# Kernel optimization log

Measured on AMD Instinct MI355X. Metric: run time of the kernel, lower is better.

The kernel has to match this reference:

```python
import jax, jax.numpy as jnp
import numpy as np

N = 8192
IN_DIM = 128
OUT_DIM = 64
ALPHA = 0.2  # leaky_relu negative slope
NEG_BIG = -9e15


def setup_inputs() -> dict:
    key = jax.random.key(0)
    k1, k2, k3, k4, k5 = jax.random.split(key, 5)
    h = jax.random.normal(k1, (N, IN_DIM), dtype=jnp.float32)
    adj = jax.random.randint(k2, (N, N), 0, 2, dtype=jnp.int32)
    w = jax.random.normal(k3, (IN_DIM, OUT_DIM), dtype=jnp.float32) * (1.414 / np.sqrt(IN_DIM))
    a = jax.random.normal(k4, (2 * OUT_DIM, 1), dtype=jnp.float32) * 0.1
    b = jax.random.uniform(k5, (OUT_DIM,), dtype=jnp.float32, minval=-1.0, maxval=1.0) / np.sqrt(OUT_DIM)
    return {"h": h, "adj": adj, "w": w, "a": a, "b": b}


def reference(h, adj, w, a, b):
    # wh: [N, D_out]
    wh = h @ w
    d = wh.shape[1]
    # broadcast attention logits: e[i,j] = leaky_relu(wh[i]@a1 + wh[j]@a2)
    wh1 = wh @ a[:d]   # [N, 1]
    wh2 = wh @ a[d:]   # [N, 1]
    e = jax.nn.leaky_relu(wh1 + wh2.T, negative_slope=ALPHA)  # [N, N]
    # adjacency mask + row softmax (dropout=0 / eval mode -> identity)
    att = jnp.where(adj > 0, e, NEG_BIG)
    att = jax.nn.softmax(att, axis=1)
    h_prime = att @ wh + b  # [N, D_out]
    return jax.nn.elu(h_prime)  # concat=True -> elu
```

## Files before the change

kernel.cpp:

```cpp
#include <hip/hip_runtime.h>
#include <hip/hip_bf16.h>

#define NN 8192
#define D_IN 128
#define D_OUT 64
#define GAT_ALPHA 0.2f
#define LOG2E 1.4426950408889634f

typedef __attribute__((ext_vector_type(4))) float f32x4;
typedef __attribute__((ext_vector_type(8))) short short8;

static __device__ __forceinline__ unsigned short f32_bf16(float f) {
    unsigned u = __builtin_bit_cast(unsigned, f);
    u += 0x7fffu + ((u >> 16) & 1u);
    return (unsigned short)(u >> 16);
}

__global__ __launch_bounds__(256) void gat_pre(
    const int* __restrict__ adj, unsigned char* __restrict__ bm,
    const float* __restrict__ h, const float* __restrict__ w,
    const float* __restrict__ a,
    unsigned short* __restrict__ whB, float* __restrict__ wh1p,
    float* __restrict__ wh2p)
{
    __shared__ float hs[16 * 128];
    __shared__ float whs[16][64];
    const int t = threadIdx.x;

    if (blockIdx.x < 2048) {
        const size_t base = (size_t)blockIdx.x * 256 + t;
        #pragma unroll
        for (int it = 0; it < 16; ++it) {
            const size_t G = (size_t)it * 524288 + base;
            const int4* p = (const int4*)(adj + G * 8);
            int4 v0 = p[0], v1 = p[1];
            unsigned b = 0;
            b |= (unsigned)(v0.x > 0) << 0;
            b |= (unsigned)(v0.y > 0) << 1;
            b |= (unsigned)(v0.z > 0) << 2;
            b |= (unsigned)(v0.w > 0) << 3;
            b |= (unsigned)(v1.x > 0) << 4;
            b |= (unsigned)(v1.y > 0) << 5;
            b |= (unsigned)(v1.z > 0) << 6;
            b |= (unsigned)(v1.w > 0) << 7;
            bm[G] = (unsigned char)b;
        }
        return;
    }

    const int i0 = (blockIdx.x - 2048) * 16;

    const float* hsrc = h + (size_t)i0 * D_IN;
    *(float4*)(hs + t * 8)     = *(const float4*)(hsrc + t * 8);
    *(float4*)(hs + t * 8 + 4) = *(const float4*)(hsrc + t * 8 + 4);
    __syncthreads();

    const int r  = t >> 4;
    const int og = (t & 15) * 4;
    f32x4 acc = {0.f, 0.f, 0.f, 0.f};
    for (int k = 0; k < D_IN; ++k) {
        float hv = hs[r * 128 + k];
        float4 wv = *(const float4*)(w + k * D_OUT + og);
        acc[0] += hv * wv.x; acc[1] += hv * wv.y;
        acc[2] += hv * wv.z; acc[3] += hv * wv.w;
    }
    whs[r][og]     = acc[0];
    whs[r][og + 1] = acc[1];
    whs[r][og + 2] = acc[2];
    whs[r][og + 3] = acc[3];

    float p1 = acc[0]*a[og] + acc[1]*a[og+1] + acc[2]*a[og+2] + acc[3]*a[og+3];
    float p2 = acc[0]*a[64+og] + acc[1]*a[64+og+1] + acc[2]*a[64+og+2] + acc[3]*a[64+og+3];
    #pragma unroll
    for (int m = 1; m < 16; m <<= 1) {
        p1 += __shfl_xor(p1, m);
        p2 += __shfl_xor(p2, m);
    }
    if ((t & 15) == 0) {
        wh1p[i0 + r] = p1 * LOG2E;
        wh2p[i0 + r] = p2 * LOG2E;
    }
    __syncthreads();

    {
        const int half = t >> 7;
        const int dim  = (t >> 1) & 63;
        const int e0   = (t & 1) * 4;
        ushort4 v;
        v.x = f32_bf16(whs[half * 8 + e0 + 0][dim]);
        v.y = f32_bf16(whs[half * 8 + e0 + 1][dim]);
        v.z = f32_bf16(whs[half * 8 + e0 + 2][dim]);
        v.w = f32_bf16(whs[half * 8 + e0 + 3][dim]);
        *(ushort4*)(whB + (size_t)(i0 / 8 + half) * 512 + dim * 8 + e0) = v;
    }
}

static __device__ __forceinline__ short8 pack8_bf16(const float* p) {
    union { unsigned int u[4]; short8 s; } r;
    asm("v_cvt_pk_bf16_f32 %0, %1, %2" : "=v"(r.u[0]) : "v"(p[0]), "v"(p[1]));
    asm("v_cvt_pk_bf16_f32 %0, %1, %2" : "=v"(r.u[1]) : "v"(p[2]), "v"(p[3]));
    asm("v_cvt_pk_bf16_f32 %0, %1, %2" : "=v"(r.u[2]) : "v"(p[4]), "v"(p[5]));
    asm("v_cvt_pk_bf16_f32 %0, %1, %2" : "=v"(r.u[3]) : "v"(p[6]), "v"(p[7]));
    return r.s;
}

__global__ __launch_bounds__(512) void gat_main(
    const unsigned int* __restrict__ bm, const unsigned short* __restrict__ whB,
    const float* __restrict__ wh1p, const float* __restrict__ wh2p,
    const float* __restrict__ bias, float* __restrict__ out)
{
    __shared__ alignas(16) char smem[66560];
    unsigned int (*bmlds)[260] = (unsigned int(*)[260])smem;
    float* w2lds = (float*)(smem + 33280);
    float (*nums)[32][64] = (float(*)[32][64])smem;
    float (*dens)[32] = (float(*)[32])(smem + 65536);

    const int t    = threadIdx.x;
    const int wv   = t >> 6;
    const int lane = t & 63;
    const int il   = lane & 15;
    const int kg   = lane >> 4;
    const int r0   = blockIdx.x * 32;

    {
        const uint4*  bmg = (const uint4*)(bm + r0 * 256);
        const float4* w2g = (const float4*)wh2p;
        #pragma unroll
        for (int q = 0; q < 4; ++q) {
            const int C = q * 512 + t;
            uint4 v = bmg[C];
            const int rr = C >> 6, cc = (C & 63) * 4;
            *(uint4*)&bmlds[rr][cc] = v;
            float4 wv2 = w2g[C];
            *(float4*)&w2lds[C * 4] = wv2;
        }
    }
    __syncthreads();

    const float c0 = wh1p[r0 + il];
    const float c1 = wh1p[r0 + 16 + il];
    const int shk = kg * 8;

    f32x4 acc[2][4] = {};
    float den0 = 0.f, den1 = 0.f;

    #pragma unroll 4
    for (int n = 0; n < 32; ++n) {
        const int jd = wv * 32 + n;
        const int j0 = jd * 32;

        unsigned int m0 = bmlds[il][jd] >> shk;
        unsigned int m1 = bmlds[16 + il][jd] >> shk;
        float4 W0 = *(const float4*)&w2lds[j0 + kg * 8];
        float4 W1 = *(const float4*)&w2lds[j0 + kg * 8 + 4];

        const unsigned short* bb = whB + (size_t)(j0 / 8 + kg) * 512 + il * 8;
        short8 b0 = *(const short8*)(bb);
        short8 b1 = *(const short8*)(bb + 128);
        short8 b2 = *(const short8*)(bb + 256);
        short8 b3 = *(const short8*)(bb + 384);

        float wvv[8] = {W0.x, W0.y, W0.z, W0.w, W1.x, W1.y, W1.z, W1.w};
        float p0[8], p1[8];
        #pragma unroll
        for (int e = 0; e < 8; ++e) {
            float x = c0 + wvv[e];
            x = fmaxf(x, GAT_ALPHA * x);
            float p = __builtin_amdgcn_exp2f(x);
            p = (m0 & (1u << e)) ? p : 0.f;
            den0 += p; p0[e] = p;
            float y = c1 + wvv[e];
            y = fmaxf(y, GAT_ALPHA * y);
            float q = __builtin_amdgcn_exp2f(y);
            q = (m1 & (1u << e)) ? q : 0.f;
            den1 += q; p1[e] = q;
        }
        short8 af0 = pack8_bf16(p0);
        short8 af1 = pack8_bf16(p1);

        acc[0][0] = __builtin_amdgcn_mfma_f32_16x16x32_bf16(af0, b0, acc[0][0], 0, 0, 0);
        acc[1][0] = __builtin_amdgcn_mfma_f32_16x16x32_bf16(af1, b0, acc[1][0], 0, 0, 0);
        acc[0][1] = __builtin_amdgcn_mfma_f32_16x16x32_bf16(af0, b1, acc[0][1], 0, 0, 0);
        acc[1][1] = __builtin_amdgcn_mfma_f32_16x16x32_bf16(af1, b1, acc[1][1], 0, 0, 0);
        acc[0][2] = __builtin_amdgcn_mfma_f32_16x16x32_bf16(af0, b2, acc[0][2], 0, 0, 0);
        acc[1][2] = __builtin_amdgcn_mfma_f32_16x16x32_bf16(af1, b2, acc[1][2], 0, 0, 0);
        acc[0][3] = __builtin_amdgcn_mfma_f32_16x16x32_bf16(af0, b3, acc[0][3], 0, 0, 0);
        acc[1][3] = __builtin_amdgcn_mfma_f32_16x16x32_bf16(af1, b3, acc[1][3], 0, 0, 0);
    }

    den0 += __shfl_xor(den0, 16); den0 += __shfl_xor(den0, 32);
    den1 += __shfl_xor(den1, 16); den1 += __shfl_xor(den1, 32);

    __syncthreads();

    if (kg == 0) { dens[wv][il] = den0; dens[wv][16 + il] = den1; }
    #pragma unroll
    for (int q = 0; q < 4; ++q) {
        #pragma unroll
        for (int d = 0; d < 4; ++d) {
            nums[wv][kg * 4 + q][d * 16 + il]      = acc[0][d][q];
            nums[wv][16 + kg * 4 + q][d * 16 + il] = acc[1][d][q];
        }
    }
    __syncthreads();

    #pragma unroll
    for (int k = 0; k < 4; ++k) {
        const int idx = k * 512 + t;
        const int rr = idx >> 6, cc = idx & 63;
        float s = 0.f, dd = 0.f;
        #pragma unroll
        for (int w8 = 0; w8 < 8; ++w8) { s += nums[w8][rr][cc]; dd += dens[w8][rr]; }
        float val = s / dd + bias[cc];
        out[(size_t)(r0 + rr) * D_OUT + cc] =
            val > 0.f ? val : (__builtin_amdgcn_exp2f(val * LOG2E) - 1.f);
    }
}

extern "C" void kernel_launch(void* const* d_in, const int* in_sizes, int n_in,
                              void* d_out, int out_size, void* d_ws, size_t ws_size,
                              hipStream_t stream) {
    const float* h   = (const float*)d_in[0];
    const int*   adj = (const int*)d_in[1];
    const float* w   = (const float*)d_in[2];
    const float* a   = (const float*)d_in[3];
    const float* b   = (const float*)d_in[4];
    float* out = (float*)d_out;

    char* ws = (char*)d_ws;
    unsigned short* whB = (unsigned short*)ws;
    float* wh1p = (float*)(ws + (size_t)D_OUT * NN * 2);
    float* wh2p = (float*)(ws + (size_t)D_OUT * NN * 2 + NN * 4);
    unsigned char* bm = (unsigned char*)(ws + (size_t)D_OUT * NN * 2 + NN * 8);

    gat_pre<<<2560, 256, 0, stream>>>(adj, bm, h, w, a, whB, wh1p, wh2p);
    gat_main<<<256, 512, 0, stream>>>((const unsigned int*)bm, whB, wh1p, wh2p, b, out);
}
```

Baseline: 79.41 us.

## Fuse adjacency bitmask packing into main attention kernel with 16-row tiles

Moves the int32 adjacency-to-bitmask conversion out of the prep kernel and into the main kernel. Each block now streams its own adjacency rows with nontemporal loads and packs them into LDS, which avoids writing and re-reading a global bitmask. The main kernel is retiled to 16 rows per block with 512 blocks, and wh2 is read straight from global memory instead of being staged in LDS. In exchange the 256MB adjacency read now sits inside the compute kernel, and whB is reused across half as many rows per block.

```diff
diff --git a/kernel.cpp b/kernel.cpp
--- a/kernel.cpp
+++ b/kernel.cpp
@@ -9,6 +9,7 @@
 
 typedef __attribute__((ext_vector_type(4))) float f32x4;
 typedef __attribute__((ext_vector_type(8))) short short8;
+typedef __attribute__((ext_vector_type(4))) int i32x4;
 
 static __device__ __forceinline__ unsigned short f32_bf16(float f) {
     unsigned u = __builtin_bit_cast(unsigned, f);
@@ -16,8 +17,7 @@
     return (unsigned short)(u >> 16);
 }
 
-__global__ __launch_bounds__(256) void gat_pre(
-    const int* __restrict__ adj, unsigned char* __restrict__ bm,
+__global__ __launch_bounds__(256) void gat_prep(
     const float* __restrict__ h, const float* __restrict__ w,
     const float* __restrict__ a,
     unsigned short* __restrict__ whB, float* __restrict__ wh1p,
@@ -26,29 +26,7 @@
     __shared__ float hs[16 * 128];
     __shared__ float whs[16][64];
     const int t = threadIdx.x;
-
-    if (blockIdx.x < 2048) {
-        const size_t base = (size_t)blockIdx.x * 256 + t;
-        #pragma unroll
-        for (int it = 0; it < 16; ++it) {
-            const size_t G = (size_t)it * 524288 + base;
-            const int4* p = (const int4*)(adj + G * 8);
-            int4 v0 = p[0], v1 = p[1];
-            unsigned b = 0;
-            b |= (unsigned)(v0.x > 0) << 0;
-            b |= (unsigned)(v0.y > 0) << 1;
-            b |= (unsigned)(v0.z > 0) << 2;
-            b |= (unsigned)(v0.w > 0) << 3;
-            b |= (unsigned)(v1.x > 0) << 4;
-            b |= (unsigned)(v1.y > 0) << 5;
-            b |= (unsigned)(v1.z > 0) << 6;
-            b |= (unsigned)(v1.w > 0) << 7;
-            bm[G] = (unsigned char)b;
-        }
-        return;
-    }
-
-    const int i0 = (blockIdx.x - 2048) * 16;
+    const int i0 = blockIdx.x * 16;
 
     const float* hsrc = h + (size_t)i0 * D_IN;
     *(float4*)(hs + t * 8)     = *(const float4*)(hsrc + t * 8);
@@ -104,45 +82,47 @@
     return r.s;
 }
 
-__global__ __launch_bounds__(512) void gat_main(
-    const unsigned int* __restrict__ bm, const unsigned short* __restrict__ whB,
+__global__ __launch_bounds__(512) void gat_fused(
+    const int* __restrict__ adj, const unsigned short* __restrict__ whB,
     const float* __restrict__ wh1p, const float* __restrict__ wh2p,
     const float* __restrict__ bias, float* __restrict__ out)
 {
-    __shared__ alignas(16) char smem[66560];
+    __shared__ alignas(16) char smem[33792];
     unsigned int (*bmlds)[260] = (unsigned int(*)[260])smem;
-    float* w2lds = (float*)(smem + 33280);
-    float (*nums)[32][64] = (float(*)[32][64])smem;
-    float (*dens)[32] = (float(*)[32])(smem + 65536);
+    float (*nums)[16][64] = (float(*)[16][64])smem;
+    float (*dens)[16] = (float(*)[16])(smem + 32768);
 
     const int t    = threadIdx.x;
     const int wv   = t >> 6;
     const int lane = t & 63;
     const int il   = lane & 15;
     const int kg   = lane >> 4;
-    const int r0   = blockIdx.x * 32;
-
-    {
-        const uint4*  bmg = (const uint4*)(bm + r0 * 256);
-        const float4* w2g = (const float4*)wh2p;
-        #pragma unroll
-        for (int q = 0; q < 4; ++q) {
-            const int C = q * 512 + t;
-            uint4 v = bmg[C];
-            const int rr = C >> 6, cc = (C & 63) * 4;
-            *(uint4*)&bmlds[rr][cc] = v;
-            float4 wv2 = w2g[C];
-            *(float4*)&w2lds[C * 4] = wv2;
+    const int r0   = blockIdx.x * 16;
+
+    for (int s = 0; s < 8; ++s) {
+        const int row = wv * 2 + (s >> 2);
+        const int p   = s & 3;
+        const i32x4* q = (const i32x4*)(adj + (size_t)(r0 + row) * NN) + p * 512 + lane * 8;
+        i32x4 v[8];
+        #pragma unroll
+        for (int k = 0; k < 8; ++k) v[k] = __builtin_nontemporal_load(q + k);
+        unsigned m = 0;
+        #pragma unroll
+        for (int k = 0; k < 8; ++k) {
+            m |= (unsigned)(v[k].x > 0) << (4 * k);
+            m |= (unsigned)(v[k].y > 0) << (4 * k + 1);
+            m |= (unsigned)(v[k].z > 0) << (4 * k + 2);
+            m |= (unsigned)(v[k].w > 0) << (4 * k + 3);
         }
-    }
-    __syncthreads();
-
-    const float c0 = wh1p[r0 + il];
-    const float c1 = wh1p[r0 + 16 + il];
+        bmlds[row][p * 64 + lane] = m;
+    }
+    __syncthreads();
+
+    const float c = wh1p[r0 + il];
     const int shk = kg * 8;
 
-    f32x4 acc[2][4] = {};
-    float den0 = 0.f, den1 = 0.f;
+    f32x4 acc0 = {0,0,0,0}, acc1 = {0,0,0,0}, acc2 = {0,0,0,0}, acc3 = {0,0,0,0};
+    float den = 0.f;
 
     #pragma unroll 4
     for (int n = 0; n < 32; ++n) {
@@ -150,9 +130,8 @@
         const int j0 = jd * 32;
 
         unsigned int m0 = bmlds[il][jd] >> shk;
-        unsigned int m1 = bmlds[16 + il][jd] >> shk;
-        float4 W0 = *(const float4*)&w2lds[j0 + kg * 8];
-        float4 W1 = *(const float4*)&w2lds[j0 + kg * 8 + 4];
+        float4 W0 = *(const float4*)(wh2p + j0 + kg * 8);
+        float4 W1 = *(const float4*)(wh2p + j0 + kg * 8 + 4);
 
         const unsigned short* bb = whB + (size_t)(j0 / 8 + kg) * 512 + il * 8;
         short8 b0 = *(const short8*)(bb);
@@ -161,51 +140,40 @@
         short8 b3 = *(const short8*)(bb + 384);
 
         float wvv[8] = {W0.x, W0.y, W0.z, W0.w, W1.x, W1.y, W1.z, W1.w};
-        float p0[8], p1[8];
+        float p0[8];
         #pragma unroll
         for (int e = 0; e < 8; ++e) {
-            float x = c0 + wvv[e];
+            float x = c + wvv[e];
             x = fmaxf(x, GAT_ALPHA * x);
             float p = __builtin_amdgcn_exp2f(x);
             p = (m0 & (1u << e)) ? p : 0.f;
-            den0 += p; p0[e] = p;
-            float y = c1 + wvv[e];
-            y = fmaxf(y, GAT_ALPHA * y);
-            float q = __builtin_amdgcn_exp2f(y);
-            q = (m1 & (1u << e)) ? q : 0.f;
-            den1 += q; p1[e] = q;
+            den += p; p0[e] = p;
         }
-        short8 af0 = pack8_bf16(p0);
-        short8 af1 = pack8_bf16(p1);
-
-        acc[0][0] = __builtin_amdgcn_mfma_f32_16x16x32_bf16(af0, b0, acc[0][0], 0, 0, 0);
-        acc[1][0] = __builtin_amdgcn_mfma_f32_16x16x32_bf16(af1, b0, acc[1][0], 0, 0, 0);
-        acc[0][1] = __builtin_amdgcn_mfma_f32_16x16x32_bf16(af0, b1, acc[0][1], 0, 0, 0);
-        acc[1][1] = __builtin_amdgcn_mfma_f32_16x16x32_bf16(af1, b1, acc[1][1], 0, 0, 0);
-        acc[0][2] = __builtin_amdgcn_mfma_f32_16x16x32_bf16(af0, b2, acc[0][2], 0, 0, 0);
-        acc[1][2] = __builtin_amdgcn_mfma_f32_16x16x32_bf16(af1, b2, acc[1][2], 0, 0, 0);
-        acc[0][3] = __builtin_amdgcn_mfma_f32_16x16x32_bf16(af0, b3, acc[0][3], 0, 0, 0);
-        acc[1][3] = __builtin_amdgcn_mfma_f32_16x16x32_bf16(af1, b3, acc[1][3], 0, 0, 0);
-    }
-
-    den0 += __shfl_xor(den0, 16); den0 += __shfl_xor(den0, 32);
-    den1 += __shfl_xor(den1, 16); den1 += __shfl_xor(den1, 32);
-
-    __syncthreads();
-
-    if (kg == 0) { dens[wv][il] = den0; dens[wv][16 + il] = den1; }
+        short8 af = pack8_bf16(p0);
+
+        acc0 = __builtin_amdgcn_mfma_f32_16x16x32_bf16(af, b0, acc0, 0, 0, 0);
+        acc1 = __builtin_amdgcn_mfma_f32_16x16x32_bf16(af, b1, acc1, 0, 0, 0);
+        acc2 = __builtin_amdgcn_mfma_f32_16x16x32_bf16(af, b2, acc2, 0, 0, 0);
+        acc3 = __builtin_amdgcn_mfma_f32_16x16x32_bf16(af, b3, acc3, 0, 0, 0);
+    }
+
+    den += __shfl_xor(den, 16);
+    den += __shfl_xor(den, 32);
+
+    __syncthreads();
+
+    if (kg == 0) dens[wv][il] = den;
     #pragma unroll
     for (int q = 0; q < 4; ++q) {
-        #pragma unroll
-        for (int d = 0; d < 4; ++d) {
-            nums[wv][kg * 4 + q][d * 16 + il]      = acc[0][d][q];
-            nums[wv][16 + kg * 4 + q][d * 16 + il] = acc[1][d][q];
-        }
+        nums[wv][kg * 4 + q][0 * 16 + il] = acc0[q];
+        nums[wv][kg * 4 + q][1 * 16 + il] = acc1[q];
+        nums[wv][kg * 4 + q][2 * 16 + il] = acc2[q];
+        nums[wv][kg * 4 + q][3 * 16 + il] = acc3[q];
     }
     __syncthreads();
 
     #pragma unroll
-    for (int k = 0; k < 4; ++k) {
+    for (int k = 0; k < 2; ++k) {
         const int idx = k * 512 + t;
         const int rr = idx >> 6, cc = idx & 63;
         float s = 0.f, dd = 0.f;
@@ -231,8 +199,7 @@
     unsigned short* whB = (unsigned short*)ws;
     float* wh1p = (float*)(ws + (size_t)D_OUT * NN * 2);
     float* wh2p = (float*)(ws + (size_t)D_OUT * NN * 2 + NN * 4);
-    unsigned char* bm = (unsigned char*)(ws + (size_t)D_OUT * NN * 2 + NN * 8);
-
-    gat_pre<<<2560, 256, 0, stream>>>(adj, bm, h, w, a, whB, wh1p, wh2p);
-    gat_main<<<256, 512, 0, stream>>>((const unsigned int*)bm, whB, wh1p, wh2p, b, out);
-}
+
+    gat_prep<<<NN / 16, 256, 0, stream>>>(h, w, a, whB, wh1p, wh2p);
+    gat_fused<<<NN / 16, 512, 0, stream>>>(adj, whB, wh1p, wh2p, b, out);
+}
```

After: 226.0 us. 185% more time.
